# Performance work log

Hardware: AMD Instinct MI355X
Metric: run time of the kernel (lower is better)

## Reference

```python
import jax, jax.numpy as jnp
import numpy as np
from jax.scipy.special import logsumexp

ITERS = 50
EPS = 0.005
B, N, D = 8, 2048, 3


def _sq_cost(x, y):
    x2 = jnp.sum(x * x, axis=-1)  # [B,N]
    y2 = jnp.sum(y * y, axis=-1)  # [B,M]
    c = x2[:, :, None] + y2[:, None, :] - 2.0 * jnp.einsum('bnd,bmd->bnm', x, y)
    return jnp.maximum(c, 0.0)


def setup_inputs() -> dict:
    key = jax.random.key(0)
    k1, k2 = jax.random.split(key)
    input1 = jax.random.normal(k1, (B, N, D), dtype=jnp.float32)
    input2 = jax.random.normal(k2, (B, N, D), dtype=jnp.float32)
    return {"input1": input1, "input2": input2}


def reference(input1, input2):
    # Approximate EMD between equal-size point sets, as in emdModule(x, y, eps, iters):
    # iterative entropic-regularized (Sinkhorn/auction-style) assignment on the
    # squared-distance cost, eps = entropic temperature, iters = sweeps.
    eps = jnp.float32(EPS)
    b, n, _ = input1.shape
    m = input2.shape[1]
    C = _sq_cost(input1, input2)  # [B,N,M]
    log_mu = -jnp.log(jnp.float32(n))
    log_nu = -jnp.log(jnp.float32(m))

    def body(carry, _):
        f, g = carry  # duals [B,N], [B,M]
        f = eps * (log_mu - logsumexp((g[:, None, :] - C) / eps, axis=2))
        g = eps * (log_nu - logsumexp((f[:, :, None] - C) / eps, axis=1))
        return (f, g), None

    f0 = jnp.zeros((b, n), dtype=C.dtype)
    g0 = jnp.zeros((b, m), dtype=C.dtype)
    (f, g), _ = jax.lax.scan(body, (f0, g0), None, length=ITERS)

    # transport plan; each row sums to 1/N (soft assignment)
    P = jnp.exp((f[:, :, None] + g[:, None, :] - C) / eps)  # [B,N,M]
    # per-point assigned squared distance (dis of emdModule), then .mean()
    dis = jnp.sum(P * C, axis=-1) * jnp.float32(n)  # [B,N]
    return jnp.mean(dis)
```

## Files before the change

kernel.cpp:

```cpp
#include <hip/hip_runtime.h>
#include <math.h>

#define NB 8
#define NN 2048
#define NM 2048
#define NITERS 50

static constexpr float F_EPS  = 0.005f;
static constexpr float LOG2E  = 1.4426950408889634f;
static constexpr float KK     = LOG2E / F_EPS;
static constexpr float TWOK   = 2.0f * KK;
static constexpr float NEG_LOG2N = -11.0f;

__device__ __forceinline__ float fexp2(float x) { return __builtin_amdgcn_exp2f(x); }
__device__ __forceinline__ float flog2(float x) { return __builtin_amdgcn_logf(x); }

__global__ void pack_init(const float* __restrict__ V, float4* __restrict__ Pout, int total)
{
    int i = blockIdx.x * blockDim.x + threadIdx.x;
    if (i < total) {
        float v0 = V[3*i], v1 = V[3*i+1], v2 = V[3*i+2];
        float s  = fmaf(v0, v0, fmaf(v1, v1, v2*v2));
        Pout[i]  = make_float4(v0, v1, v2, -KK * s);
    }
}

__global__ __launch_bounds__(256, 4) void sink_update(
    const float4* __restrict__ Pin,
    const float*  __restrict__ Vraw,
    float4*       __restrict__ Pout)
{
    __shared__ float2 part [16][129];
    __shared__ float2 part2[16][17];
    const int tid  = threadIdx.x;
    const int lane = tid & 63;
    const int wave = tid >> 6;
    const int rw   = wave & 1;
    const int mh   = wave >> 1;
    const int wgs_per_b = NN / 16;
    const int b       = blockIdx.x / wgs_per_b;
    const int rowbase = (blockIdx.x % wgs_per_b) * 16;

    float xs0[8], xs1[8], xs2[8];
    {
        const float* vb = Vraw + ((size_t)(b * NN + rowbase + rw * 8)) * 3;
        #pragma unroll
        for (int r = 0; r < 8; ++r) {
            xs0[r] = TWOK * vb[r*3+0];
            xs1[r] = TWOK * vb[r*3+1];
            xs2[r] = TWOK * vb[r*3+2];
        }
    }

    const float4* __restrict__ pp = Pin + b * NM + mh * 1024 + lane;

    float rm[8], rs[8];
    #pragma unroll
    for (int r = 0; r < 8; ++r) { rm[r] = -1e30f; rs[r] = 0.f; }

    float4 c0 = pp[0*64], c1 = pp[1*64], c2 = pp[2*64], c3 = pp[3*64];

    #pragma unroll
    for (int ib = 0; ib < 4; ++ib) {
        float4 n0, n1, n2, n3;
        if (ib < 3) {
            n0 = pp[(ib*4 + 4) * 64];
            n1 = pp[(ib*4 + 5) * 64];
            n2 = pp[(ib*4 + 6) * 64];
            n3 = pp[(ib*4 + 7) * 64];
        }
        #pragma unroll
        for (int r = 0; r < 8; ++r) {
            const float z0 = fmaf(xs0[r], c0.x, fmaf(xs1[r], c0.y, fmaf(xs2[r], c0.z, c0.w)));
            const float z1 = fmaf(xs0[r], c1.x, fmaf(xs1[r], c1.y, fmaf(xs2[r], c1.z, c1.w)));
            const float z2 = fmaf(xs0[r], c2.x, fmaf(xs1[r], c2.y, fmaf(xs2[r], c2.z, c2.w)));
            const float z3 = fmaf(xs0[r], c3.x, fmaf(xs1[r], c3.y, fmaf(xs2[r], c3.z, c3.w)));
            const float cm = fmaxf(fmaxf(z0, z1), fmaxf(z2, z3));
            const float nm = fmaxf(rm[r], cm);
            const float s  = (fexp2(z0 - nm) + fexp2(z1 - nm))
                           + (fexp2(z2 - nm) + fexp2(z3 - nm));
            rs[r] = fmaf(rs[r], fexp2(rm[r] - nm), s);
            rm[r] = nm;
        }
        if (ib < 3) { c0 = n0; c1 = n1; c2 = n2; c3 = n3; }
    }

    #pragma unroll
    for (int r = 0; r < 8; ++r)
        part[rw*8 + r][mh*64 + lane] = make_float2(rm[r], rs[r]);
    __syncthreads();

    {
        const int row = tid & 15, seg = tid >> 4;
        float m8 = -1e30f;
        float2 v[8];
        #pragma unroll
        for (int k = 0; k < 8; ++k) { v[k] = part[row][seg*8 + k]; m8 = fmaxf(m8, v[k].x); }
        float s8 = 0.f;
        #pragma unroll
        for (int k = 0; k < 8; ++k) s8 = fmaf(v[k].y, fexp2(v[k].x - m8), s8);
        part2[row][seg] = make_float2(m8, s8);
    }
    __syncthreads();

    if (tid < 16) {
        float gm = -1e30f;
        float2 v[16];
        #pragma unroll
        for (int k = 0; k < 16; ++k) { v[k] = part2[tid][k]; gm = fmaxf(gm, v[k].x); }
        float s = 0.f;
        #pragma unroll
        for (int k = 0; k < 16; ++k) s = fmaf(v[k].y, fexp2(v[k].x - gm), s);
        const float lse2 = gm + flog2(s);
        const int n0 = rowbase + tid;
        const float* vp = Vraw + ((size_t)(b * NN + n0)) * 3;
        Pout[b * NN + n0] = make_float4(vp[0], vp[1], vp[2], NEG_LOG2N - lse2);
    }
}

__global__ __launch_bounds__(256, 4) void final_loss(
    const float4* __restrict__ Px, const float4* __restrict__ Py,
    float* __restrict__ out)
{
    __shared__ float wsum[4];
    const int tid  = threadIdx.x;
    const int lane = tid & 63;
    const int wave = tid >> 6;
    const int rw   = wave & 1;
    const int mh   = wave >> 1;
    const int wgs_per_b = NN / 16;
    const int b       = blockIdx.x / wgs_per_b;
    const int rowbase = (blockIdx.x % wgs_per_b) * 16;

    float xr0[8], xr1[8], xr2[8], Af[8], xq[8];
    {
        const float4* xb = Px + b * NN + rowbase + rw * 8;
        #pragma unroll
        for (int r = 0; r < 8; ++r) {
            const float4 xp = xb[r];
            xr0[r] = xp.x; xr1[r] = xp.y; xr2[r] = xp.z; Af[r] = xp.w;
            xq[r]  = fmaf(xp.x, xp.x, fmaf(xp.y, xp.y, xp.z * xp.z));
        }
    }

    const float4* __restrict__ pp = Py + b * NM + mh * 1024 + lane;

    float acc = 0.f;
    float4 cur = pp[0];
    #pragma unroll
    for (int i = 0; i < 16; ++i) {
        float4 nxt;
        if (i < 15) nxt = pp[(i + 1) * 64];
        const float ysq = fmaf(cur.x, cur.x, fmaf(cur.y, cur.y, cur.z * cur.z));
        #pragma unroll
        for (int r = 0; r < 8; ++r) {
            const float dot = fmaf(xr0[r], cur.x, fmaf(xr1[r], cur.y, xr2[r] * cur.z));
            const float cc  = fmaxf(fmaf(-2.f, dot, xq[r] + ysq), 0.f);
            const float zp  = fmaf(TWOK, dot, Af[r] + cur.w);
            acc = fmaf(fexp2(zp), cc, acc);
        }
        if (i < 15) cur = nxt;
    }
    #pragma unroll
    for (int o = 32; o > 0; o >>= 1) acc += __shfl_xor(acc, o);
    if (lane == 0) wsum[wave] = acc;
    __syncthreads();
    if (tid == 0) {
        atomicAdd(out, (wsum[0] + wsum[1] + wsum[2] + wsum[3]) * (1.0f / NB));
    }
}

extern "C" void kernel_launch(void* const* d_in, const int* in_sizes, int n_in,
                              void* d_out, int out_size, void* d_ws, size_t ws_size,
                              hipStream_t stream)
{
    const float* x = (const float*)d_in[0];
    const float* y = (const float*)d_in[1];
    float4* Px = (float4*)d_ws;
    float4* Py = Px + NB * NN;

    pack_init<<<(NB * NM + 255) / 256, 256, 0, stream>>>(y, Py, NB * NM);

    for (int it = 0; it < NITERS; ++it) {
        sink_update<<<NB * NN / 16, 256, 0, stream>>>(Py, x, Px);
        sink_update<<<NB * NM / 16, 256, 0, stream>>>(Px, y, Py);
    }

    hipMemsetAsync(d_out, 0, sizeof(float), stream);
    final_loss<<<NB * NN / 16, 256, 0, stream>>>(Px, Py, (float*)d_out);
}
```

Baseline: 1.120 ms.

## Give each wave all 16 rows over a quarter of the columns

The work split changes so each of the four waves handles all 16 rows against a 512-column slice, instead of 8 rows against a 1024-column slice. Each loaded column point is now reused across twice as many rows, halving global loads per row, and the LDS partial buffer is widened to hold 256 entries per row. The explicit register double-buffering of the next column chunk is removed and left to the compiler. Register pressure rises from 16-element per-row arrays, which may hurt occupancy under the launch bounds of 4, and the second reduction stage now merges 16 partials per thread instead of 8.

Measured after the change: 1.121 ms. About the same (+0.1%).

```diff
diff --git a/kernel.cpp b/kernel.cpp
--- a/kernel.cpp
+++ b/kernel.cpp
@@ -30,47 +30,40 @@
     const float*  __restrict__ Vraw,
     float4*       __restrict__ Pout)
 {
-    __shared__ float2 part [16][129];
+    __shared__ float2 part [16][257];
     __shared__ float2 part2[16][17];
     const int tid  = threadIdx.x;
     const int lane = tid & 63;
     const int wave = tid >> 6;
-    const int rw   = wave & 1;
-    const int mh   = wave >> 1;
     const int wgs_per_b = NN / 16;
     const int b       = blockIdx.x / wgs_per_b;
     const int rowbase = (blockIdx.x % wgs_per_b) * 16;
 
-    float xs0[8], xs1[8], xs2[8];
+    float xs0[16], xs1[16], xs2[16];
     {
-        const float* vb = Vraw + ((size_t)(b * NN + rowbase + rw * 8)) * 3;
+        const float* vb = Vraw + ((size_t)(b * NN + rowbase)) * 3;
         #pragma unroll
-        for (int r = 0; r < 8; ++r) {
+        for (int r = 0; r < 16; ++r) {
             xs0[r] = TWOK * vb[r*3+0];
             xs1[r] = TWOK * vb[r*3+1];
             xs2[r] = TWOK * vb[r*3+2];
         }
     }
 
-    const float4* __restrict__ pp = Pin + b * NM + mh * 1024 + lane;
+    const float4* __restrict__ pp = Pin + b * NM + wave * 512 + lane;
 
-    float rm[8], rs[8];
+    float rm[16], rs[16];
     #pragma unroll
-    for (int r = 0; r < 8; ++r) { rm[r] = -1e30f; rs[r] = 0.f; }
-
-    float4 c0 = pp[0*64], c1 = pp[1*64], c2 = pp[2*64], c3 = pp[3*64];
+    for (int r = 0; r < 16; ++r) { rm[r] = -1e30f; rs[r] = 0.f; }
 
     #pragma unroll
-    for (int ib = 0; ib < 4; ++ib) {
-        float4 n0, n1, n2, n3;
-        if (ib < 3) {
-            n0 = pp[(ib*4 + 4) * 64];
-            n1 = pp[(ib*4 + 5) * 64];
-            n2 = pp[(ib*4 + 6) * 64];
-            n3 = pp[(ib*4 + 7) * 64];
-        }
+    for (int ib = 0; ib < 2; ++ib) {
+        const float4 c0 = pp[(ib*4 + 0) * 64];
+        const float4 c1 = pp[(ib*4 + 1) * 64];
+        const float4 c2 = pp[(ib*4 + 2) * 64];
+        const float4 c3 = pp[(ib*4 + 3) * 64];
         #pragma unroll
-        for (int r = 0; r < 8; ++r) {
+        for (int r = 0; r < 16; ++r) {
             const float z0 = fmaf(xs0[r], c0.x, fmaf(xs1[r], c0.y, fmaf(xs2[r], c0.z, c0.w)));
             const float z1 = fmaf(xs0[r], c1.x, fmaf(xs1[r], c1.y, fmaf(xs2[r], c1.z, c1.w)));
             const float z2 = fmaf(xs0[r], c2.x, fmaf(xs1[r], c2.y, fmaf(xs2[r], c2.z, c2.w)));
@@ -82,24 +75,23 @@
             rs[r] = fmaf(rs[r], fexp2(rm[r] - nm), s);
             rm[r] = nm;
         }
-        if (ib < 3) { c0 = n0; c1 = n1; c2 = n2; c3 = n3; }
     }
 
     #pragma unroll
-    for (int r = 0; r < 8; ++r)
-        part[rw*8 + r][mh*64 + lane] = make_float2(rm[r], rs[r]);
+    for (int r = 0; r < 16; ++r)
+        part[r][tid] = make_float2(rm[r], rs[r]);
     __syncthreads();
 
     {
         const int row = tid & 15, seg = tid >> 4;
-        float m8 = -1e30f;
-        float2 v[8];
+        float m16 = -1e30f;
+        float2 v[16];
         #pragma unroll
-        for (int k = 0; k < 8; ++k) { v[k] = part[row][seg*8 + k]; m8 = fmaxf(m8, v[k].x); }
-        float s8 = 0.f;
+        for (int k = 0; k < 16; ++k) { v[k] = part[row][seg*16 + k]; m16 = fmaxf(m16, v[k].x); }
+        float s16 = 0.f;
         #pragma unroll
-        for (int k = 0; k < 8; ++k) s8 = fmaf(v[k].y, fexp2(v[k].x - m8), s8);
-        part2[row][seg] = make_float2(m8, s8);
+        for (int k = 0; k < 16; ++k) s16 = fmaf(v[k].y, fexp2(v[k].x - m16), s16);
+        part2[row][seg] = make_float2(m16, s16);
     }
     __syncthreads();
 
@@ -126,40 +118,35 @@
     const int tid  = threadIdx.x;
     const int lane = tid & 63;
     const int wave = tid >> 6;
-    const int rw   = wave & 1;
-    const int mh   = wave >> 1;
     const int wgs_per_b = NN / 16;
     const int b       = blockIdx.x / wgs_per_b;
     const int rowbase = (blockIdx.x % wgs_per_b) * 16;
 
-    float xr0[8], xr1[8], xr2[8], Af[8], xq[8];
+    float xr0[16], xr1[16], xr2[16], Af[16], xq[16];
     {
-        const float4* xb = Px + b * NN + rowbase + rw * 8;
+        const float4* xb = Px + b * NN + rowbase;
         #pragma unroll
-        for (int r = 0; r < 8; ++r) {
+        for (int r = 0; r < 16; ++r) {
             const float4 xp = xb[r];
             xr0[r] = xp.x; xr1[r] = xp.y; xr2[r] = xp.z; Af[r] = xp.w;
             xq[r]  = fmaf(xp.x, xp.x, fmaf(xp.y, xp.y, xp.z * xp.z));
         }
     }
 
-    const float4* __restrict__ pp = Py + b * NM + mh * 1024 + lane;
+    const float4* __restrict__ pp = Py + b * NM + wave * 512 + lane;
 
     float acc = 0.f;
-    float4 cur = pp[0];
     #pragma unroll
-    for (int i = 0; i < 16; ++i) {
-        float4 nxt;
-        if (i < 15) nxt = pp[(i + 1) * 64];
-        const float ysq = fmaf(cur.x, cur.x, fmaf(cur.y, cur.y, cur.z * cur.z));
+    for (int i = 0; i < 8; ++i) {
+        const float4 p = pp[i * 64];
+        const float ysq = fmaf(p.x, p.x, fmaf(p.y, p.y, p.z * p.z));
         #pragma unroll
-        for (int r = 0; r < 8; ++r) {
-            const float dot = fmaf(xr0[r], cur.x, fmaf(xr1[r], cur.y, xr2[r] * cur.z));
+        for (int r = 0; r < 16; ++r) {
+            const float dot = fmaf(xr0[r], p.x, fmaf(xr1[r], p.y, xr2[r] * p.z));
             const float cc  = fmaxf(fmaf(-2.f, dot, xq[r] + ysq), 0.f);
-            const float zp  = fmaf(TWOK, dot, Af[r] + cur.w);
+            const float zp  = fmaf(TWOK, dot, Af[r] + p.w);
             acc = fmaf(fexp2(zp), cc, acc);
         }
-        if (i < 15) cur = nxt;
     }
     #pragma unroll
     for (int o = 32; o > 0; o >>= 1) acc += __shfl_xor(acc, o);
```
